# Kernel tuning notes

Measured on AMD Instinct MI355X. Metric: run time of the kernel, lower is better.

Reference implementation:

```python
import jax, jax.numpy as jnp
import numpy as np

NDIM = (256, 256, 256)
NMIN = (-1.0, -1.0, -1.0)
NMAX = (1.0, 1.0, 1.0)
NDELTA = tuple((NMAX[i] - NMIN[i]) / (NDIM[i] - 1.0) for i in range(3))
MIN_DEG, MAX_DEG = 0, 10
ANNEALED_ALPHA = 1.0
EPS = 1e-12


def compute_grad(grid):
    # central differences on the voxel grid with edge padding -> [N, 3]
    g = grid.reshape(NDIM[0], NDIM[1], NDIM[2])
    p = jnp.pad(g, ((1, 1), (1, 1), (1, 1)), mode='edge')
    dx = (p[2:, 1:-1, 1:-1] - p[:-2, 1:-1, 1:-1]) / (2.0 * NDELTA[0])
    dy = (p[1:-1, 2:, 1:-1] - p[1:-1, :-2, 1:-1]) / (2.0 * NDELTA[1])
    dz = (p[1:-1, 1:-1, 2:] - p[1:-1, 1:-1, :-2]) / (2.0 * NDELTA[2])
    return jnp.stack([dx, dy, dz], axis=-1).reshape(-1, 3)


def trilinear3(data, pts):
    # data: [N, 4] flattened voxel features, pts: [B, 3] -> [B, 4]
    x = (pts[..., 0] - NMIN[0]) / NDELTA[0]
    y = (pts[..., 1] - NMIN[1]) / NDELTA[1]
    z = (pts[..., 2] - NMIN[2]) / NDELTA[2]
    x0f = jnp.floor(x); y0f = jnp.floor(y); z0f = jnp.floor(z)
    xd = (x - x0f)[..., None]
    yd = (y - y0f)[..., None]
    zd = (z - z0f)[..., None]
    x0 = jnp.clip(x0f.astype(jnp.int32), 0, NDIM[0] - 1)
    x1 = jnp.clip(x0f.astype(jnp.int32) + 1, 0, NDIM[0] - 1)
    y0 = jnp.clip(y0f.astype(jnp.int32), 0, NDIM[1] - 1)
    y1 = jnp.clip(y0f.astype(jnp.int32) + 1, 0, NDIM[1] - 1)
    z0 = jnp.clip(z0f.astype(jnp.int32), 0, NDIM[2] - 1)
    z1 = jnp.clip(z0f.astype(jnp.int32) + 1, 0, NDIM[2] - 1)
    sYZ, sZ = NDIM[1] * NDIM[2], NDIM[2]
    gat = lambda i, j, k: data[sYZ * i + sZ * j + k]
    c00 = gat(x0, y0, z0) * (1 - xd) + gat(x1, y0, z0) * xd
    c01 = gat(x0, y0, z1) * (1 - xd) + gat(x1, y0, z1) * xd
    c10 = gat(x0, y1, z0) * (1 - xd) + gat(x1, y1, z0) * xd
    c11 = gat(x0, y1, z1) * (1 - xd) + gat(x1, y1, z1) * xd
    c0 = c00 * (1 - yd) + c10 * yd
    c1 = c01 * (1 - yd) + c11 * yd
    return c0 * (1 - zd) + c1 * zd


def annealed_pos_enc(x, alpha):
    # nerfies-style windowed positional encoding with identity concat
    bands = jnp.arange(MIN_DEG, MAX_DEG, dtype=x.dtype)  # [D]
    scales = 2.0 ** bands
    xb = x[..., None, :] * scales[:, None]               # [..., D, 3]
    four = jnp.sin(jnp.stack([xb, xb + 0.5 * jnp.pi], axis=-2))  # [..., D, 2, 3]
    w = jnp.clip(alpha - bands, 0.0, 1.0)
    w = 0.5 * (1.0 - jnp.cos(jnp.pi * w))                # cosine easing window
    four = four * w[:, None, None]
    four = four.reshape(x.shape[:-1] + (-1,))            # [..., D*6]
    return jnp.concatenate([x, four], axis=-1)           # [..., 3 + D*6]


def mlp(feats, w0, b0, w1, b1, w2, b2, w3, b3, wo, bo):
    # net_depth=4, skip_layer=2 -> concat inputs after layer index 2
    h = jax.nn.relu(feats @ w0 + b0)
    h = jax.nn.relu(h @ w1 + b1)
    h = jax.nn.relu(h @ w2 + b2)
    h = jnp.concatenate([h, feats], axis=-1)
    h = jax.nn.relu(h @ w3 + b3)
    return h @ wo + bo


def safe_l2_norm(v):
    return jnp.sqrt(jnp.sum(v * v, axis=-1, keepdims=True) + EPS)


def setup_inputs() -> dict:
    key = jax.random.key(0)
    ks = jax.random.split(key, 8)
    B = 1048576
    N = NDIM[0] * NDIM[1] * NDIM[2]
    x = jax.random.uniform(ks[0], (B, 3), jnp.float32, -1.0, 1.0)
    grid = jax.random.normal(ks[1], (N, 1), jnp.float32)
    glorot = lambda k, fi, fo: jax.random.normal(k, (fi, fo), jnp.float32) * jnp.sqrt(2.0 / (fi + fo))
    return {
        'x': x, 'grid': grid,
        'w0': glorot(ks[2], 63, 128), 'b0': jnp.zeros((128,), jnp.float32),
        'w1': glorot(ks[3], 128, 128), 'b1': jnp.zeros((128,), jnp.float32),
        'w2': glorot(ks[4], 128, 128), 'b2': jnp.zeros((128,), jnp.float32),
        'w3': glorot(ks[5], 191, 128), 'b3': jnp.zeros((128,), jnp.float32),
        'wo': jax.random.normal(ks[6], (128, 3), jnp.float32) * 1e-5,  # output_init normal(1e-5)
        'bo': jnp.zeros((3,), jnp.float32),
    }


def reference(x, grid, w0, b0, w1, b1, w2, b2, w3, b3, wo, bo):
    data = jnp.concatenate([grid, compute_grad(grid)], axis=-1)  # [N, 4]
    ret = trilinear3(data, x)                                    # [B, 4]
    feats = annealed_pos_enc(x[:, None], ANNEALED_ALPHA * MAX_DEG)  # [B, 1, 63]
    raw = mlp(feats, w0, b0, w1, b1, w2, b2, w3, b3, wo, bo)[:, 0]  # [B, 3]
    # residual + direct output: rotate gradient vector by axis-angle raw
    theta = safe_l2_norm(raw)
    e = raw / theta
    cond = ret[..., 1:]
    a = safe_l2_norm(cond)
    v = cond / a
    rot = a * (jnp.cos(theta) * v + jnp.sin(theta) * jnp.cross(e, v)
               + (1.0 - jnp.cos(theta)) * jnp.sum(e * v, axis=-1, keepdims=True) * e)
    return (ret[..., :1], ret[..., 1:], rot)
```

## Files before the change

kernel.cpp:

```cpp
#include <hip/hip_runtime.h>


typedef __attribute__((ext_vector_type(4))) float f4;
typedef long long llg;
typedef __attribute__((ext_vector_type(2))) long long llg2;

#define MFMA8 __builtin_amdgcn_mfma_f32_16x16x32_fp8_fp8

__device__ __forceinline__ float bf2f(unsigned int u) {
    union { float f; unsigned int i; } v; v.i = u << 16; return v.f;
}
__device__ __forceinline__ unsigned int pkbf(float a, float b) {
    unsigned int r;
    asm("v_cvt_pk_bf16_f32 %0, %1, %2" : "=v"(r) : "v"(a), "v"(b));
    return r;
}
__device__ __forceinline__ float vfract(float a) {
    float d; asm("v_fract_f32 %0, %1" : "=v"(d) : "v"(a)); return d;
}
__device__ __forceinline__ float vsin(float a) {
    float d; asm("v_sin_f32 %0, %1" : "=v"(d) : "v"(a)); return d;
}
__device__ __forceinline__ float gv(const float* __restrict__ g, int i, int j, int k) {
    return g[(i * 256 + j) * 256 + k];
}
__device__ __forceinline__ int featmap(int kp) {
    if (kp < 3) return kp;
    if (kp == 3) return -1;
    const int m = kp - 4, b = m / 6, r = m - 6 * b, d = r >> 1, c = r & 1;
    return 3 + 6 * b + 3 * c + d;
}
__device__ __forceinline__ int hidperm(int k) {
    const int kt = k >> 5, q = (k >> 3) & 3, j = k & 7;
    return 32 * kt + ((j >> 2) << 4) + (q << 2) + (j & 3);
}
__device__ __forceinline__ llg mkllg(unsigned int lo, unsigned int hi) {
    return (llg)(((unsigned long long)lo) | (((unsigned long long)hi) << 32));
}
__device__ __forceinline__ unsigned int pack8(f4 acc) {
    int d = __builtin_amdgcn_cvt_pk_fp8_f32(fmaxf(acc[0], 0.f), fmaxf(acc[1], 0.f), 0, false);
    d     = __builtin_amdgcn_cvt_pk_fp8_f32(fmaxf(acc[2], 0.f), fmaxf(acc[3], 0.f), d, true);
    return (unsigned int)d;
}

#define WS_TOTAL 67584
#define SWZ_BLOCKS 264
#define DG_BLOCKS 8192
#define DG_OFF_SH 131072
#define WS_NEED (262144ull + 16777216ull * 8ull)
#define WO_SCALE 8192.0f
#define WO_INV   (1.0f / 8192.0f)

__global__ __launch_bounds__(256) void prep(
    const float* __restrict__ g,
    const float* __restrict__ w0, const float* __restrict__ w1,
    const float* __restrict__ w2, const float* __restrict__ w3,
    const float* __restrict__ wo,
    unsigned char* __restrict__ ws8, unsigned short* __restrict__ dg,
    int do_dgrid)
{
    const int bid = blockIdx.x;
    if (bid < SWZ_BLOCKS) {
        int idx = bid * 256 + threadIdx.x;
        const float* src; int base, KTP, Kact, Nact, ld;
        if (idx < 8192)       { src = w0; base = 0;     KTP = 1; Kact = 64;  Nact = 128; ld = 128; }
        else if (idx < 24576) { src = w1; base = 8192;  KTP = 2; Kact = 128; Nact = 128; ld = 128; }
        else if (idx < 40960) { src = w2; base = 24576; KTP = 2; Kact = 128; Nact = 128; ld = 128; }
        else if (idx < 65536) { src = w3; base = 40960; KTP = 3; Kact = 192; Nact = 128; ld = 128; }
        else                  { src = wo; base = 65536; KTP = 2; Kact = 128; Nact = 3;   ld = 3;   }
        int local = idx - base;
        int j    = local & 7;
        int half = (local >> 3) & 1;
        int lane = (local >> 4) & 63;
        int c    = local >> 10;
        int ktp  = c % KTP, nt = c / KTP;
        int kt   = ktp * 2 + half;
        int k = kt * 32 + ((lane >> 4) << 3) + j;
        int n = nt * 16 + (lane & 15);
        float v = 0.0f;
        if (k < Kact && n < Nact) {
            int ko;
            if (base == 0) {
                ko = featmap(k);
            } else if (base == 40960) {
                if (k >= 128) {
                    int f = featmap(k - 128);
                    ko = (f < 0) ? -1 : 128 + f;
                } else {
                    ko = hidperm(k);
                }
            } else {
                ko = hidperm(k);
            }
            if (ko >= 0) v = src[ko * ld + n];
            if (base == 65536) v *= WO_SCALE;
        }
        int p = __builtin_amdgcn_cvt_pk_fp8_f32(v, v, 0, false);
        ws8[idx] = (unsigned char)(p & 0xff);
    } else if (do_dgrid) {
        const int t  = (bid - SWZ_BLOCKS) * 256 + threadIdx.x;
        const int k0 = (t & 31) << 3;
        const int j  = (t >> 5) & 255;
        const int i  = t >> 13;
        const float* row = g + (i * 256 + j) * 256;
        const float* rxp = g + (min(i + 1, 255) * 256 + j) * 256;
        const float* rxm = g + (max(i - 1, 0)   * 256 + j) * 256;
        const float* ryp = g + (i * 256 + min(j + 1, 255)) * 256;
        const float* rym = g + (i * 256 + max(j - 1, 0))   * 256;
        float se[8], sxp[8], sxm[8], syp[8], sym[8];
        {
            f4 a = *(const f4*)(row + k0), b = *(const f4*)(row + k0 + 4);
            #pragma unroll
            for (int q = 0; q < 4; ++q) { se[q] = a[q]; se[q + 4] = b[q]; }
            a = *(const f4*)(rxp + k0); b = *(const f4*)(rxp + k0 + 4);
            #pragma unroll
            for (int q = 0; q < 4; ++q) { sxp[q] = a[q]; sxp[q + 4] = b[q]; }
            a = *(const f4*)(rxm + k0); b = *(const f4*)(rxm + k0 + 4);
            #pragma unroll
            for (int q = 0; q < 4; ++q) { sxm[q] = a[q]; sxm[q + 4] = b[q]; }
            a = *(const f4*)(ryp + k0); b = *(const f4*)(ryp + k0 + 4);
            #pragma unroll
            for (int q = 0; q < 4; ++q) { syp[q] = a[q]; syp[q + 4] = b[q]; }
            a = *(const f4*)(rym + k0); b = *(const f4*)(rym + k0 + 4);
            #pragma unroll
            for (int q = 0; q < 4; ++q) { sym[q] = a[q]; sym[q + 4] = b[q]; }
        }
        float zv[10];
        zv[0] = row[max(k0 - 1, 0)];
        #pragma unroll
        for (int q = 0; q < 8; ++q) zv[q + 1] = se[q];
        zv[9] = row[min(k0 + 8, 255)];
        unsigned int o[16];
        #pragma unroll
        for (int q = 0; q < 8; ++q) {
            o[q * 2 + 0] = pkbf(se[q], (sxp[q] - sxm[q]) * 63.75f);
            o[q * 2 + 1] = pkbf((syp[q] - sym[q]) * 63.75f, (zv[q + 2] - zv[q]) * 63.75f);
        }
        unsigned short* dst = dg + (size_t)(((i * 256 + j) * 256 + k0)) * 4;
        #pragma unroll
        for (int q = 0; q < 4; ++q)
            *(uint4*)(dst + q * 8) = *(const uint4*)(&o[q * 4]);
    }
}

#define FSTRIDE_B 88
#define WV_BYTES (32 * FSTRIDE_B)

#define HIDDEN_LAYER(WSL, BIASP, SRCP, DSTP)                                    \
    do {                                                                        \
        _Pragma("unroll")                                                       \
        for (int utp = 0; utp < 4; ++utp) {                                     \
            const int utA = 2 * utp, utB = 2 * utp + 1;                         \
            llg2 wa0 = *(const llg2*)((WSL) + ((utA * 2 + 0) * 64 + lane) * 16);\
            llg2 wa1 = *(const llg2*)((WSL) + ((utA * 2 + 1) * 64 + lane) * 16);\
            llg2 wb0 = *(const llg2*)((WSL) + ((utB * 2 + 0) * 64 + lane) * 16);\
            llg2 wb1 = *(const llg2*)((WSL) + ((utB * 2 + 1) * 64 + lane) * 16);\
            const f4 biasA = *(const f4*)((BIASP) + utA * 16 + quad * 4);       \
            const f4 biasB = *(const f4*)((BIASP) + utB * 16 + quad * 4);       \
            _Pragma("unroll")                                                   \
            for (int pt = 0; pt < 2; ++pt) {                                    \
                f4 a0 = biasA, a1 = biasB;                                      \
                a0 = MFMA8(wa0[0], SRCP[pt][0], a0, 0, 0, 0);                   \
                a0 = MFMA8(wa0[1], SRCP[pt][1], a0, 0, 0, 0);                   \
                a0 = MFMA8(wa1[0], SRCP[pt][2], a0, 0, 0, 0);                   \
                a0 = MFMA8(wa1[1], SRCP[pt][3], a0, 0, 0, 0);                   \
                a1 = MFMA8(wb0[0], SRCP[pt][0], a1, 0, 0, 0);                   \
                a1 = MFMA8(wb0[1], SRCP[pt][1], a1, 0, 0, 0);                   \
                a1 = MFMA8(wb1[0], SRCP[pt][2], a1, 0, 0, 0);                   \
                a1 = MFMA8(wb1[1], SRCP[pt][3], a1, 0, 0, 0);                   \
                DSTP[pt][utp] = mkllg(pack8(a0), pack8(a1));                    \
            }                                                                   \
        }                                                                       \
    } while (0)

template<bool FAST>
__global__ __launch_bounds__(256, 5) void voxmlp(
    const float* __restrict__ x, const float* __restrict__ grid,
    const unsigned char* __restrict__ ws8, const unsigned short* __restrict__ dg,
    const float* __restrict__ b0, const float* __restrict__ b1,
    const float* __restrict__ b2, const float* __restrict__ b3,
    const float* __restrict__ bo,
    float* __restrict__ out, int B)
{
    __shared__ unsigned char smem[WV_BYTES * 4];

    const int lane = threadIdx.x & 63;
    const int wave = threadIdx.x >> 6;
    const int quad = lane >> 4;
    const int lm   = lane & 15;
    unsigned char* fbuf = smem + wave * WV_BYTES;

    const int pbase = blockIdx.x * 128 + wave * 32;

    const int p2   = lane & 31;
    const int role = lane >> 5;
    const int pid  = pbase + p2;

    const float px = x[pid * 3 + 0];
    const float py = x[pid * 3 + 1];
    const float pz = x[pid * 3 + 2];

    if (role == 0) {
        const float fx = (px + 1.0f) * 127.5f;
        const float fy = (py + 1.0f) * 127.5f;
        const float fz = (pz + 1.0f) * 127.5f;
        const float fx0 = floorf(fx), fy0 = floorf(fy), fz0 = floorf(fz);
        const float xd = fx - fx0, yd = fy - fy0, zd = fz - fz0;
        const int ix0 = min(max((int)fx0, 0), 255);
        const int iy0 = min(max((int)fy0, 0), 255);
        const int iz0 = min(max((int)fz0, 0), 255);
        const int ix1 = min(ix0 + 1, 255);
        const int iy1 = min(iy0 + 1, 255);
        const int iz1 = min(iz0 + 1, 255);

        float ret0 = 0.f, c1 = 0.f, c2 = 0.f, c3 = 0.f;
        if (FAST) {
            const unsigned char* dgb = (const unsigned char*)dg;
            const unsigned int vbase = (unsigned int)((ix0 * 65536 + iy0 * 256 + iz0) << 3);
            const unsigned int ox = (unsigned int)((ix1 - ix0) << 19);
            const unsigned int oy = (unsigned int)((iy1 - iy0) << 11);
            const unsigned int oz = (unsigned int)((iz1 - iz0) << 3);
            #pragma unroll
            for (int c = 0; c < 8; ++c) {
                const float wgt = ((c & 4) ? xd : 1.0f - xd) *
                                  ((c & 2) ? yd : 1.0f - yd) *
                                  ((c & 1) ? zd : 1.0f - zd);
                const unsigned int off = vbase + ((c & 4) ? ox : 0u)
                                               + ((c & 2) ? oy : 0u)
                                               + ((c & 1) ? oz : 0u);
                const uint2 w = *(const uint2*)(dgb + off);
                ret0 = fmaf(wgt, bf2f(w.x & 0xffffu), ret0);
                c1   = fmaf(wgt, bf2f(w.x >> 16),     c1);
                c2   = fmaf(wgt, bf2f(w.y & 0xffffu), c2);
                c3   = fmaf(wgt, bf2f(w.y >> 16),     c3);
            }
        } else {
            #pragma unroll
            for (int c = 0; c < 8; ++c) {
                const int i = (c & 4) ? ix1 : ix0;
                const int j = (c & 2) ? iy1 : iy0;
                const int k = (c & 1) ? iz1 : iz0;
                const float wgt = ((c & 4) ? xd : 1.0f - xd) *
                                  ((c & 2) ? yd : 1.0f - yd) *
                                  ((c & 1) ? zd : 1.0f - zd);
                const float v  = gv(grid, i, j, k);
                const float gx = (gv(grid, min(i + 1, 255), j, k) - gv(grid, max(i - 1, 0), j, k)) * 63.75f;
                const float gy = (gv(grid, i, min(j + 1, 255), k) - gv(grid, i, max(j - 1, 0), k)) * 63.75f;
                const float gz = (gv(grid, i, j, min(k + 1, 255)) - gv(grid, i, j, max(k - 1, 0))) * 63.75f;
                ret0 = fmaf(wgt, v,  ret0);
                c1   = fmaf(wgt, gx, c1);
                c2   = fmaf(wgt, gy, c2);
                c3   = fmaf(wgt, gz, c3);
            }
        }
        out[pid] = ret0;
        out[B + pid * 3 + 0] = c1;
        out[B + pid * 3 + 1] = c2;
        out[B + pid * 3 + 2] = c3;
        float* cst = (float*)(fbuf + p2 * FSTRIDE_B + 64);
        cst[0] = c1; cst[1] = c2; cst[2] = c3;
    } else {
        float s[64];
        s[0] = px; s[1] = py; s[2] = pz; s[3] = 0.0f;
        float r0 = px * 0.15915494309189535f;
        float r1 = py * 0.15915494309189535f;
        float r2 = pz * 0.15915494309189535f;
        #pragma unroll
        for (int b = 0; b < 10; ++b) {
            s[4 + b * 6 + 0] = vsin(vfract(r0));
            s[4 + b * 6 + 1] = vsin(vfract(r0 + 0.25f));
            s[4 + b * 6 + 2] = vsin(vfract(r1));
            s[4 + b * 6 + 3] = vsin(vfract(r1 + 0.25f));
            s[4 + b * 6 + 4] = vsin(vfract(r2));
            s[4 + b * 6 + 5] = vsin(vfract(r2 + 0.25f));
            r0 += r0; r1 += r1; r2 += r2;
        }
        unsigned int dw[16];
        #pragma unroll
        for (int i = 0; i < 16; ++i) {
            int d = __builtin_amdgcn_cvt_pk_fp8_f32(s[4 * i + 0], s[4 * i + 1], 0, false);
            d     = __builtin_amdgcn_cvt_pk_fp8_f32(s[4 * i + 2], s[4 * i + 3], d, true);
            dw[i] = (unsigned int)d;
        }
        unsigned char* fb = fbuf + p2 * FSTRIDE_B;
        #pragma unroll
        for (int i = 0; i < 8; ++i) {
            uint2 pk; pk.x = dw[2 * i]; pk.y = dw[2 * i + 1];
            *(uint2*)(fb + i * 8) = pk;
        }
    }
    __builtin_amdgcn_s_barrier();

    const int frow0 = lm * FSTRIDE_B + quad * 8;

    llg actA[2][4];
    llg actB[2][4];
    llg ffp[2][2];

    #pragma unroll
    for (int pt = 0; pt < 2; ++pt)
        #pragma unroll
        for (int kt = 0; kt < 2; ++kt)
            ffp[pt][kt] = *(const llg*)(fbuf + pt * 16 * FSTRIDE_B + frow0 + kt * 32);

    #pragma unroll
    for (int utp = 0; utp < 4; ++utp) {
        const int utA = 2 * utp, utB = 2 * utp + 1;
        llg2 wA = *(const llg2*)(ws8 + (utA * 64 + lane) * 16);
        llg2 wB = *(const llg2*)(ws8 + (utB * 64 + lane) * 16);
        const f4 biasA = *(const f4*)(b0 + utA * 16 + quad * 4);
        const f4 biasB = *(const f4*)(b0 + utB * 16 + quad * 4);
        #pragma unroll
        for (int pt = 0; pt < 2; ++pt) {
            f4 a0 = biasA, a1 = biasB;
            a0 = MFMA8(wA[0], ffp[pt][0], a0, 0, 0, 0);
            a0 = MFMA8(wA[1], ffp[pt][1], a0, 0, 0, 0);
            a1 = MFMA8(wB[0], ffp[pt][0], a1, 0, 0, 0);
            a1 = MFMA8(wB[1], ffp[pt][1], a1, 0, 0, 0);
            actA[pt][utp] = mkllg(pack8(a0), pack8(a1));
        }
    }

    HIDDEN_LAYER(ws8 + 8192,  b1, actA, actB);
    HIDDEN_LAYER(ws8 + 24576, b2, actB, actA);

    #pragma unroll
    for (int utp = 0; utp < 4; ++utp) {
        const int utA = 2 * utp, utB = 2 * utp + 1;
        llg2 ha0 = *(const llg2*)(ws8 + 40960 + ((utA * 3 + 0) * 64 + lane) * 16);
        llg2 ha1 = *(const llg2*)(ws8 + 40960 + ((utA * 3 + 1) * 64 + lane) * 16);
        llg2 ha2 = *(const llg2*)(ws8 + 40960 + ((utA * 3 + 2) * 64 + lane) * 16);
        llg2 hb0 = *(const llg2*)(ws8 + 40960 + ((utB * 3 + 0) * 64 + lane) * 16);
        llg2 hb1 = *(const llg2*)(ws8 + 40960 + ((utB * 3 + 1) * 64 + lane) * 16);
        llg2 hb2 = *(const llg2*)(ws8 + 40960 + ((utB * 3 + 2) * 64 + lane) * 16);
        const f4 biasA = *(const f4*)(b3 + utA * 16 + quad * 4);
        const f4 biasB = *(const f4*)(b3 + utB * 16 + quad * 4);
        #pragma unroll
        for (int pt = 0; pt < 2; ++pt) {
            f4 a0 = biasA, a1 = biasB;
            a0 = MFMA8(ha0[0], actA[pt][0], a0, 0, 0, 0);
            a0 = MFMA8(ha0[1], actA[pt][1], a0, 0, 0, 0);
            a0 = MFMA8(ha1[0], actA[pt][2], a0, 0, 0, 0);
            a0 = MFMA8(ha1[1], actA[pt][3], a0, 0, 0, 0);
            a0 = MFMA8(ha2[0], ffp[pt][0],  a0, 0, 0, 0);
            a0 = MFMA8(ha2[1], ffp[pt][1],  a0, 0, 0, 0);
            a1 = MFMA8(hb0[0], actA[pt][0], a1, 0, 0, 0);
            a1 = MFMA8(hb0[1], actA[pt][1], a1, 0, 0, 0);
            a1 = MFMA8(hb1[0], actA[pt][2], a1, 0, 0, 0);
            a1 = MFMA8(hb1[1], actA[pt][3], a1, 0, 0, 0);
            a1 = MFMA8(hb2[0], ffp[pt][0],  a1, 0, 0, 0);
            a1 = MFMA8(hb2[1], ffp[pt][1],  a1, 0, 0, 0);
            actB[pt][utp] = mkllg(pack8(a0), pack8(a1));
        }
    }

    llg2 o0 = *(const llg2*)(ws8 + 65536 + ((0 * 64 + lane) * 16));
    llg2 o1 = *(const llg2*)(ws8 + 65536 + ((1 * 64 + lane) * 16) + 64 * 16 * 0);
    o1 = *(const llg2*)(ws8 + 65536 + ((64 + lane) * 16));

    const float bo0 = bo[0], bo1 = bo[1], bo2 = bo[2];
    #pragma unroll
    for (int pt = 0; pt < 2; ++pt) {
        f4 acc = {0.f, 0.f, 0.f, 0.f};
        acc = MFMA8(o0[0], actB[pt][0], acc, 0, 0, 0);
        acc = MFMA8(o0[1], actB[pt][1], acc, 0, 0, 0);
        acc = MFMA8(o1[0], actB[pt][2], acc, 0, 0, 0);
        acc = MFMA8(o1[1], actB[pt][3], acc, 0, 0, 0);

        const int pp = pt * 16 + lm;
        const float* cst = (const float*)(fbuf + pp * FSTRIDE_B + 64);
        const float g1 = cst[0], g2 = cst[1], g3 = cst[2];
        const float r0 = acc[0] * WO_INV + bo0;
        const float r1 = acc[1] * WO_INV + bo1;
        const float r2 = acc[2] * WO_INV + bo2;
        const float theta = sqrtf(fmaf(r0, r0, fmaf(r1, r1, r2 * r2)) + 1e-12f);
        const float it = __builtin_amdgcn_rcpf(theta);
        const float e0 = r0 * it, e1 = r1 * it, e2 = r2 * it;
        const float a = sqrtf(fmaf(g1, g1, fmaf(g2, g2, g3 * g3)) + 1e-12f);
        const float ia = __builtin_amdgcn_rcpf(a);
        const float v0 = g1 * ia, v1 = g2 * ia, v2 = g3 * ia;
        float st, ct;
        __sincosf(theta, &st, &ct);
        const float cx = e1 * v2 - e2 * v1;
        const float cy = e2 * v0 - e0 * v2;
        const float cz = e0 * v1 - e1 * v0;
        const float om = (1.0f - ct) * (e0 * v0 + e1 * v1 + e2 * v2);
        if (quad == 0) {
            const int pid2 = pbase + pp;
            out[4 * B + pid2 * 3 + 0] = a * (ct * v0 + st * cx + om * e0);
            out[4 * B + pid2 * 3 + 1] = a * (ct * v1 + st * cy + om * e1);
            out[4 * B + pid2 * 3 + 2] = a * (ct * v2 + st * cz + om * e2);
        }
    }
}

extern "C" void kernel_launch(void* const* d_in, const int* in_sizes, int n_in,
                              void* d_out, int out_size, void* d_ws, size_t ws_size,
                              hipStream_t stream)
{
    const float* x    = (const float*)d_in[0];
    const float* grid = (const float*)d_in[1];
    const float* w0   = (const float*)d_in[2];
    const float* b0   = (const float*)d_in[3];
    const float* w1   = (const float*)d_in[4];
    const float* b1   = (const float*)d_in[5];
    const float* w2   = (const float*)d_in[6];
    const float* b2   = (const float*)d_in[7];
    const float* w3   = (const float*)d_in[8];
    const float* b3   = (const float*)d_in[9];
    const float* wo   = (const float*)d_in[10];
    const float* bo   = (const float*)d_in[11];
    float* out = (float*)d_out;
    unsigned char* ws8 = (unsigned char*)d_ws;
    unsigned short* dg = (unsigned short*)d_ws + DG_OFF_SH;

    const int B = in_sizes[0] / 3;
    const int fast = (ws_size >= WS_NEED) ? 1 : 0;
    const int nprep = fast ? (SWZ_BLOCKS + DG_BLOCKS) : SWZ_BLOCKS;
    prep<<<nprep, 256, 0, stream>>>(grid, w0, w1, w2, w3, wo, ws8, dg, fast);
    if (fast)
        voxmlp<true><<<B / 128, 256, 0, stream>>>(x, grid, ws8, dg, b0, b1, b2, b3, bo, out, B);
    else
        voxmlp<false><<<B / 128, 256, 0, stream>>>(x, grid, ws8, dg, b0, b1, b2, b3, bo, out, B);
}
```

Baseline: 335.4 us.

## Process MLP one 16-point tile at a time to cut registers, raise occupancy

Restructures the fused MLP so each wave runs all layers for one 16-point sub-tile before moving to the next, instead of holding activations for both sub-tiles at once. This halves the live activation registers, allowing launch bounds to request 6 waves per SIMD instead of 5. Weight fragments are now reloaded for each sub-tile, doubling weight loads from cache. Positional-encoding slots are computed on the fly during packing, and the final sincos uses hardware v_sin with fract.

```diff
diff --git a/kernel.cpp b/kernel.cpp
--- a/kernel.cpp
+++ b/kernel.cpp
@@ -50,6 +50,7 @@
 #define WS_NEED (262144ull + 16777216ull * 8ull)
 #define WO_SCALE 8192.0f
 #define WO_INV   (1.0f / 8192.0f)
+#define INV2PI 0.15915494309189535f
 
 __global__ __launch_bounds__(256) void prep(
     const float* __restrict__ g,
@@ -146,35 +147,8 @@
 #define FSTRIDE_B 88
 #define WV_BYTES (32 * FSTRIDE_B)
 
-#define HIDDEN_LAYER(WSL, BIASP, SRCP, DSTP)                                    \
-    do {                                                                        \
-        _Pragma("unroll")                                                       \
-        for (int utp = 0; utp < 4; ++utp) {                                     \
-            const int utA = 2 * utp, utB = 2 * utp + 1;                         \
-            llg2 wa0 = *(const llg2*)((WSL) + ((utA * 2 + 0) * 64 + lane) * 16);\
-            llg2 wa1 = *(const llg2*)((WSL) + ((utA * 2 + 1) * 64 + lane) * 16);\
-            llg2 wb0 = *(const llg2*)((WSL) + ((utB * 2 + 0) * 64 + lane) * 16);\
-            llg2 wb1 = *(const llg2*)((WSL) + ((utB * 2 + 1) * 64 + lane) * 16);\
-            const f4 biasA = *(const f4*)((BIASP) + utA * 16 + quad * 4);       \
-            const f4 biasB = *(const f4*)((BIASP) + utB * 16 + quad * 4);       \
-            _Pragma("unroll")                                                   \
-            for (int pt = 0; pt < 2; ++pt) {                                    \
-                f4 a0 = biasA, a1 = biasB;                                      \
-                a0 = MFMA8(wa0[0], SRCP[pt][0], a0, 0, 0, 0);                   \
-                a0 = MFMA8(wa0[1], SRCP[pt][1], a0, 0, 0, 0);                   \
-                a0 = MFMA8(wa1[0], SRCP[pt][2], a0, 0, 0, 0);                   \
-                a0 = MFMA8(wa1[1], SRCP[pt][3], a0, 0, 0, 0);                   \
-                a1 = MFMA8(wb0[0], SRCP[pt][0], a1, 0, 0, 0);                   \
-                a1 = MFMA8(wb0[1], SRCP[pt][1], a1, 0, 0, 0);                   \
-                a1 = MFMA8(wb1[0], SRCP[pt][2], a1, 0, 0, 0);                   \
-                a1 = MFMA8(wb1[1], SRCP[pt][3], a1, 0, 0, 0);                   \
-                DSTP[pt][utp] = mkllg(pack8(a0), pack8(a1));                    \
-            }                                                                   \
-        }                                                                       \
-    } while (0)
-
 template<bool FAST>
-__global__ __launch_bounds__(256, 5) void voxmlp(
+__global__ __launch_bounds__(256, 6) void voxmlp(
     const float* __restrict__ x, const float* __restrict__ grid,
     const unsigned char* __restrict__ ws8, const unsigned short* __restrict__ dg,
     const float* __restrict__ b0, const float* __restrict__ b1,
@@ -246,7 +220,7 @@
                 const float v  = gv(grid, i, j, k);
                 const float gx = (gv(grid, min(i + 1, 255), j, k) - gv(grid, max(i - 1, 0), j, k)) * 63.75f;
                 const float gy = (gv(grid, i, min(j + 1, 255), k) - gv(grid, i, max(j - 1, 0), k)) * 63.75f;
-                const float gz = (gv(grid, i, j, min(k + 1, 255)) - gv(grid, i, j, max(k - 1, 0))) * 63.75f;
+                const float gz = (gv(grid, i, j, min(k + 1, 255)) - gv(grid, i, j, min(k - 1, 0) >= 0 ? max(k - 1, 0) : 0)) * 63.75f;
                 ret0 = fmaf(wgt, v,  ret0);
                 c1   = fmaf(wgt, gx, c1);
                 c2   = fmaf(wgt, gy, c2);
@@ -260,136 +234,154 @@
         float* cst = (float*)(fbuf + p2 * FSTRIDE_B + 64);
         cst[0] = c1; cst[1] = c2; cst[2] = c3;
     } else {
-        float s[64];
-        s[0] = px; s[1] = py; s[2] = pz; s[3] = 0.0f;
-        float r0 = px * 0.15915494309189535f;
-        float r1 = py * 0.15915494309189535f;
-        float r2 = pz * 0.15915494309189535f;
-        #pragma unroll
-        for (int b = 0; b < 10; ++b) {
-            s[4 + b * 6 + 0] = vsin(vfract(r0));
-            s[4 + b * 6 + 1] = vsin(vfract(r0 + 0.25f));
-            s[4 + b * 6 + 2] = vsin(vfract(r1));
-            s[4 + b * 6 + 3] = vsin(vfract(r1 + 0.25f));
-            s[4 + b * 6 + 4] = vsin(vfract(r2));
-            s[4 + b * 6 + 5] = vsin(vfract(r2 + 0.25f));
-            r0 += r0; r1 += r1; r2 += r2;
-        }
-        unsigned int dw[16];
-        #pragma unroll
-        for (int i = 0; i < 16; ++i) {
-            int d = __builtin_amdgcn_cvt_pk_fp8_f32(s[4 * i + 0], s[4 * i + 1], 0, false);
-            d     = __builtin_amdgcn_cvt_pk_fp8_f32(s[4 * i + 2], s[4 * i + 3], d, true);
-            dw[i] = (unsigned int)d;
-        }
+        const float r0 = px * INV2PI, r1 = py * INV2PI, r2 = pz * INV2PI;
         unsigned char* fb = fbuf + p2 * FSTRIDE_B;
-        #pragma unroll
-        for (int i = 0; i < 8; ++i) {
-            uint2 pk; pk.x = dw[2 * i]; pk.y = dw[2 * i + 1];
-            *(uint2*)(fb + i * 8) = pk;
+        auto slotv = [&](int n) -> float {
+            if (n == 0) return px;
+            if (n == 1) return py;
+            if (n == 2) return pz;
+            if (n == 3) return 0.0f;
+            const int m = n - 4, b = m / 6, t = m % 6, ax = t >> 1, ph = t & 1;
+            const float rr = (ax == 0) ? r0 : (ax == 1) ? r1 : r2;
+            const float arg = rr * (float)(1 << b) + (ph ? 0.25f : 0.0f);
+            return vsin(vfract(arg));
+        };
+        #pragma unroll
+        for (int w = 0; w < 8; ++w) {
+            int lo = __builtin_amdgcn_cvt_pk_fp8_f32(slotv(8 * w + 0), slotv(8 * w + 1), 0, false);
+            lo     = __builtin_amdgcn_cvt_pk_fp8_f32(slotv(8 * w + 2), slotv(8 * w + 3), lo, true);
+            int hi = __builtin_amdgcn_cvt_pk_fp8_f32(slotv(8 * w + 4), slotv(8 * w + 5), 0, false);
+            hi     = __builtin_amdgcn_cvt_pk_fp8_f32(slotv(8 * w + 6), slotv(8 * w + 7), hi, true);
+            uint2 pk; pk.x = (unsigned int)lo; pk.y = (unsigned int)hi;
+            *(uint2*)(fb + w * 8) = pk;
         }
     }
     __builtin_amdgcn_s_barrier();
 
     const int frow0 = lm * FSTRIDE_B + quad * 8;
-
-    llg actA[2][4];
-    llg actB[2][4];
-    llg ffp[2][2];
-
-    #pragma unroll
-    for (int pt = 0; pt < 2; ++pt)
-        #pragma unroll
-        for (int kt = 0; kt < 2; ++kt)
-            ffp[pt][kt] = *(const llg*)(fbuf + pt * 16 * FSTRIDE_B + frow0 + kt * 32);
-
-    #pragma unroll
-    for (int utp = 0; utp < 4; ++utp) {
-        const int utA = 2 * utp, utB = 2 * utp + 1;
-        llg2 wA = *(const llg2*)(ws8 + (utA * 64 + lane) * 16);
-        llg2 wB = *(const llg2*)(ws8 + (utB * 64 + lane) * 16);
-        const f4 biasA = *(const f4*)(b0 + utA * 16 + quad * 4);
-        const f4 biasB = *(const f4*)(b0 + utB * 16 + quad * 4);
-        #pragma unroll
-        for (int pt = 0; pt < 2; ++pt) {
-            f4 a0 = biasA, a1 = biasB;
-            a0 = MFMA8(wA[0], ffp[pt][0], a0, 0, 0, 0);
-            a0 = MFMA8(wA[1], ffp[pt][1], a0, 0, 0, 0);
-            a1 = MFMA8(wB[0], ffp[pt][0], a1, 0, 0, 0);
-            a1 = MFMA8(wB[1], ffp[pt][1], a1, 0, 0, 0);
-            actA[pt][utp] = mkllg(pack8(a0), pack8(a1));
-        }
-    }
-
-    HIDDEN_LAYER(ws8 + 8192,  b1, actA, actB);
-    HIDDEN_LAYER(ws8 + 24576, b2, actB, actA);
-
-    #pragma unroll
-    for (int utp = 0; utp < 4; ++utp) {
-        const int utA = 2 * utp, utB = 2 * utp + 1;
-        llg2 ha0 = *(const llg2*)(ws8 + 40960 + ((utA * 3 + 0) * 64 + lane) * 16);
-        llg2 ha1 = *(const llg2*)(ws8 + 40960 + ((utA * 3 + 1) * 64 + lane) * 16);
-        llg2 ha2 = *(const llg2*)(ws8 + 40960 + ((utA * 3 + 2) * 64 + lane) * 16);
-        llg2 hb0 = *(const llg2*)(ws8 + 40960 + ((utB * 3 + 0) * 64 + lane) * 16);
-        llg2 hb1 = *(const llg2*)(ws8 + 40960 + ((utB * 3 + 1) * 64 + lane) * 16);
-        llg2 hb2 = *(const llg2*)(ws8 + 40960 + ((utB * 3 + 2) * 64 + lane) * 16);
-        const f4 biasA = *(const f4*)(b3 + utA * 16 + quad * 4);
-        const f4 biasB = *(const f4*)(b3 + utB * 16 + quad * 4);
-        #pragma unroll
-        for (int pt = 0; pt < 2; ++pt) {
-            f4 a0 = biasA, a1 = biasB;
-            a0 = MFMA8(ha0[0], actA[pt][0], a0, 0, 0, 0);
-            a0 = MFMA8(ha0[1], actA[pt][1], a0, 0, 0, 0);
-            a0 = MFMA8(ha1[0], actA[pt][2], a0, 0, 0, 0);
-            a0 = MFMA8(ha1[1], actA[pt][3], a0, 0, 0, 0);
-            a0 = MFMA8(ha2[0], ffp[pt][0],  a0, 0, 0, 0);
-            a0 = MFMA8(ha2[1], ffp[pt][1],  a0, 0, 0, 0);
-            a1 = MFMA8(hb0[0], actA[pt][0], a1, 0, 0, 0);
-            a1 = MFMA8(hb0[1], actA[pt][1], a1, 0, 0, 0);
-            a1 = MFMA8(hb1[0], actA[pt][2], a1, 0, 0, 0);
-            a1 = MFMA8(hb1[1], actA[pt][3], a1, 0, 0, 0);
-            a1 = MFMA8(hb2[0], ffp[pt][0],  a1, 0, 0, 0);
-            a1 = MFMA8(hb2[1], ffp[pt][1],  a1, 0, 0, 0);
-            actB[pt][utp] = mkllg(pack8(a0), pack8(a1));
-        }
-    }
-
-    llg2 o0 = *(const llg2*)(ws8 + 65536 + ((0 * 64 + lane) * 16));
-    llg2 o1 = *(const llg2*)(ws8 + 65536 + ((1 * 64 + lane) * 16) + 64 * 16 * 0);
-    o1 = *(const llg2*)(ws8 + 65536 + ((64 + lane) * 16));
-
     const float bo0 = bo[0], bo1 = bo[1], bo2 = bo[2];
+
     #pragma unroll
     for (int pt = 0; pt < 2; ++pt) {
-        f4 acc = {0.f, 0.f, 0.f, 0.f};
-        acc = MFMA8(o0[0], actB[pt][0], acc, 0, 0, 0);
-        acc = MFMA8(o0[1], actB[pt][1], acc, 0, 0, 0);
-        acc = MFMA8(o1[0], actB[pt][2], acc, 0, 0, 0);
-        acc = MFMA8(o1[1], actB[pt][3], acc, 0, 0, 0);
-
-        const int pp = pt * 16 + lm;
-        const float* cst = (const float*)(fbuf + pp * FSTRIDE_B + 64);
-        const float g1 = cst[0], g2 = cst[1], g3 = cst[2];
-        const float r0 = acc[0] * WO_INV + bo0;
-        const float r1 = acc[1] * WO_INV + bo1;
-        const float r2 = acc[2] * WO_INV + bo2;
-        const float theta = sqrtf(fmaf(r0, r0, fmaf(r1, r1, r2 * r2)) + 1e-12f);
-        const float it = __builtin_amdgcn_rcpf(theta);
-        const float e0 = r0 * it, e1 = r1 * it, e2 = r2 * it;
-        const float a = sqrtf(fmaf(g1, g1, fmaf(g2, g2, g3 * g3)) + 1e-12f);
-        const float ia = __builtin_amdgcn_rcpf(a);
-        const float v0 = g1 * ia, v1 = g2 * ia, v2 = g3 * ia;
-        float st, ct;
-        __sincosf(theta, &st, &ct);
-        const float cx = e1 * v2 - e2 * v1;
-        const float cy = e2 * v0 - e0 * v2;
-        const float cz = e0 * v1 - e1 * v0;
-        const float om = (1.0f - ct) * (e0 * v0 + e1 * v1 + e2 * v2);
-        if (quad == 0) {
-            const int pid2 = pbase + pp;
-            out[4 * B + pid2 * 3 + 0] = a * (ct * v0 + st * cx + om * e0);
-            out[4 * B + pid2 * 3 + 1] = a * (ct * v1 + st * cy + om * e1);
-            out[4 * B + pid2 * 3 + 2] = a * (ct * v2 + st * cz + om * e2);
+        const llg ffp0 = *(const llg*)(fbuf + pt * 16 * FSTRIDE_B + frow0);
+        const llg ffp1 = *(const llg*)(fbuf + pt * 16 * FSTRIDE_B + frow0 + 32);
+
+        llg actA[4];
+        llg actB[4];
+
+        #pragma unroll
+        for (int utp = 0; utp < 4; ++utp) {
+            const llg2 wA = *(const llg2*)(ws8 + ((2 * utp) * 64 + lane) * 16);
+            const llg2 wB = *(const llg2*)(ws8 + ((2 * utp + 1) * 64 + lane) * 16);
+            f4 a0 = *(const f4*)(b0 + (2 * utp) * 16 + quad * 4);
+            f4 a1 = *(const f4*)(b0 + (2 * utp + 1) * 16 + quad * 4);
+            a0 = MFMA8(wA[0], ffp0, a0, 0, 0, 0);
+            a0 = MFMA8(wA[1], ffp1, a0, 0, 0, 0);
+            a1 = MFMA8(wB[0], ffp0, a1, 0, 0, 0);
+            a1 = MFMA8(wB[1], ffp1, a1, 0, 0, 0);
+            actA[utp] = mkllg(pack8(a0), pack8(a1));
+        }
+
+        #pragma unroll
+        for (int utp = 0; utp < 4; ++utp) {
+            const unsigned char* wsl = ws8 + 8192;
+            const llg2 wa0 = *(const llg2*)(wsl + (((2 * utp) * 2 + 0) * 64 + lane) * 16);
+            const llg2 wa1 = *(const llg2*)(wsl + (((2 * utp) * 2 + 1) * 64 + lane) * 16);
+            const llg2 wb0 = *(const llg2*)(wsl + (((2 * utp + 1) * 2 + 0) * 64 + lane) * 16);
+            const llg2 wb1 = *(const llg2*)(wsl + (((2 * utp + 1) * 2 + 1) * 64 + lane) * 16);
+            f4 a0 = *(const f4*)(b1 + (2 * utp) * 16 + quad * 4);
+            f4 a1 = *(const f4*)(b1 + (2 * utp + 1) * 16 + quad * 4);
+            a0 = MFMA8(wa0[0], actA[0], a0, 0, 0, 0);
+            a0 = MFMA8(wa0[1], actA[1], a0, 0, 0, 0);
+            a0 = MFMA8(wa1[0], actA[2], a0, 0, 0, 0);
+            a0 = MFMA8(wa1[1], actA[3], a0, 0, 0, 0);
+            a1 = MFMA8(wb0[0], actA[0], a1, 0, 0, 0);
+            a1 = MFMA8(wb0[1], actA[1], a1, 0, 0, 0);
+            a1 = MFMA8(wb1[0], actA[2], a1, 0, 0, 0);
+            a1 = MFMA8(wb1[1], actA[3], a1, 0, 0, 0);
+            actB[utp] = mkllg(pack8(a0), pack8(a1));
+        }
+
+        #pragma unroll
+        for (int utp = 0; utp < 4; ++utp) {
+            const unsigned char* wsl = ws8 + 24576;
+            const llg2 wa0 = *(const llg2*)(wsl + (((2 * utp) * 2 + 0) * 64 + lane) * 16);
+            const llg2 wa1 = *(const llg2*)(wsl + (((2 * utp) * 2 + 1) * 64 + lane) * 16);
+            const llg2 wb0 = *(const llg2*)(wsl + (((2 * utp + 1) * 2 + 0) * 64 + lane) * 16);
+            const llg2 wb1 = *(const llg2*)(wsl + (((2 * utp + 1) * 2 + 1) * 64 + lane) * 16);
+            f4 a0 = *(const f4*)(b2 + (2 * utp) * 16 + quad * 4);
+            f4 a1 = *(const f4*)(b2 + (2 * utp + 1) * 16 + quad * 4);
+            a0 = MFMA8(wa0[0], actB[0], a0, 0, 0, 0);
+            a0 = MFMA8(wa0[1], actB[1], a0, 0, 0, 0);
+            a0 = MFMA8(wa1[0], actB[2], a0, 0, 0, 0);
+            a0 = MFMA8(wa1[1], actB[3], a0, 0, 0, 0);
+            a1 = MFMA8(wb0[0], actB[0], a1, 0, 0, 0);
+            a1 = MFMA8(wb0[1], actB[1], a1, 0, 0, 0);
+            a1 = MFMA8(wb1[0], actB[2], a1, 0, 0, 0);
+            a1 = MFMA8(wb1[1], actB[3], a1, 0, 0, 0);
+            actA[utp] = mkllg(pack8(a0), pack8(a1));
+        }
+
+        #pragma unroll
+        for (int utp = 0; utp < 4; ++utp) {
+            const unsigned char* wsl = ws8 + 40960;
+            llg hA[6], hB[6];
+            #pragma unroll
+            for (int kt = 0; kt < 6; ++kt) {
+                hA[kt] = *(const llg*)(wsl + (((2 * utp) * 3 + (kt >> 1)) * 64 + lane) * 16 + (kt & 1) * 8);
+                hB[kt] = *(const llg*)(wsl + (((2 * utp + 1) * 3 + (kt >> 1)) * 64 + lane) * 16 + (kt & 1) * 8);
+            }
+            f4 a0 = *(const f4*)(b3 + (2 * utp) * 16 + quad * 4);
+            f4 a1 = *(const f4*)(b3 + (2 * utp + 1) * 16 + quad * 4);
+            a0 = MFMA8(hA[0], actA[0], a0, 0, 0, 0);
+            a0 = MFMA8(hA[1], actA[1], a0, 0, 0, 0);
+            a0 = MFMA8(hA[2], actA[2], a0, 0, 0, 0);
+            a0 = MFMA8(hA[3], actA[3], a0, 0, 0, 0);
+            a0 = MFMA8(hA[4], ffp0,    a0, 0, 0, 0);
+            a0 = MFMA8(hA[5], ffp1,    a0, 0, 0, 0);
+            a1 = MFMA8(hB[0], actA[0], a1, 0, 0, 0);
+            a1 = MFMA8(hB[1], actA[1], a1, 0, 0, 0);
+            a1 = MFMA8(hB[2], actA[2], a1, 0, 0, 0);
+            a1 = MFMA8(hB[3], actA[3], a1, 0, 0, 0);
+            a1 = MFMA8(hB[4], ffp0,    a1, 0, 0, 0);
+            a1 = MFMA8(hB[5], ffp1,    a1, 0, 0, 0);
+            actB[utp] = mkllg(pack8(a0), pack8(a1));
+        }
+
+        {
+            const llg2 o0 = *(const llg2*)(ws8 + 65536 + (lane * 16));
+            const llg2 o1 = *(const llg2*)(ws8 + 65536 + ((64 + lane) * 16));
+            f4 acc = {0.f, 0.f, 0.f, 0.f};
+            acc = MFMA8(o0[0], actB[0], acc, 0, 0, 0);
+            acc = MFMA8(o0[1], actB[1], acc, 0, 0, 0);
+            acc = MFMA8(o1[0], actB[2], acc, 0, 0, 0);
+            acc = MFMA8(o1[1], actB[3], acc, 0, 0, 0);
+
+            const int pp = pt * 16 + lm;
+            const float* cst = (const float*)(fbuf + pp * FSTRIDE_B + 64);
+            const float g1 = cst[0], g2 = cst[1], g3 = cst[2];
+            const float r0 = acc[0] * WO_INV + bo0;
+            const float r1 = acc[1] * WO_INV + bo1;
+            const float r2 = acc[2] * WO_INV + bo2;
+            const float theta = sqrtf(fmaf(r0, r0, fmaf(r1, r1, r2 * r2)) + 1e-12f);
+            const float it = __builtin_amdgcn_rcpf(theta);
+            const float e0 = r0 * it, e1 = r1 * it, e2 = r2 * it;
+            const float a = sqrtf(fmaf(g1, g1, fmaf(g2, g2, g3 * g3)) + 1e-12f);
+            const float ia = __builtin_amdgcn_rcpf(a);
+            const float v0 = g1 * ia, v1 = g2 * ia, v2 = g3 * ia;
+            const float rv = theta * INV2PI;
+            const float st = vsin(vfract(rv));
+            const float ct = vsin(vfract(rv + 0.25f));
+            const float cx = e1 * v2 - e2 * v1;
+            const float cy = e2 * v0 - e0 * v2;
+            const float cz = e0 * v1 - e1 * v0;
+            const float om = (1.0f - ct) * (e0 * v0 + e1 * v1 + e2 * v2);
+            if (quad == 0) {
+                const int pid2 = pbase + pp;
+                out[4 * B + pid2 * 3 + 0] = a * (ct * v0 + st * cx + om * e0);
+                out[4 * B + pid2 * 3 + 1] = a * (ct * v1 + st * cy + om * e1);
+                out[4 * B + pid2 * 3 + 2] = a * (ct * v2 + st * cz + om * e2);
+            }
         }
     }
 }
```

Result: slower. 598.3 us (+78.4%).
